# Performance work log

Hardware: AMD Instinct MI355X
Metric: run time of the kernel (lower is better)

## Reference

```python
import jax, jax.numpy as jnp
import numpy as np

B, N, F, E, C, FC = 16, 5000, 512, 160000, 64, 128


def gcn_conv(x, src, dst, W, b, n_total):
    loop = jnp.arange(n_total, dtype=src.dtype)
    s = jnp.concatenate([src, loop])
    d = jnp.concatenate([dst, loop])
    deg = jax.ops.segment_sum(jnp.ones_like(s, dtype=x.dtype), d, num_segments=n_total)
    dinv = jnp.where(deg > 0, jax.lax.rsqrt(deg), 0.0)
    norm = dinv[s] * dinv[d]                      # [E']
    h = x @ W                                      # [n_total, out]
    msg = h[s] * norm[:, None]
    out = jax.ops.segment_sum(msg, d, num_segments=n_total)
    return out + b


def setup_inputs() -> dict:
    key = jax.random.key(0)
    ks = jax.random.split(key, 12)
    inp = {
        "node_features": jax.random.normal(ks[0], (B, N, F), jnp.float32),
        "col_features": jax.random.normal(ks[1], (B, C, FC), jnp.float32),
        "edge_index": jax.random.randint(ks[2], (2, E), 0, N, dtype=jnp.int64),
        # GCNConv 1/2 weights + node head
        "W1": jax.random.normal(ks[3], (F, 16), jnp.float32) / np.sqrt(F),
        "b1": jnp.zeros((16,), jnp.float32),
        "W2": jax.random.normal(ks[4], (16, 16), jnp.float32) / 4.0,
        "b2": jnp.zeros((16,), jnp.float32),
        "fc_w": jax.random.normal(ks[5], (16, 1), jnp.float32) / 4.0,
        "fc_b": jnp.zeros((1,), jnp.float32),
        # column MLP: Linear(FC,16) -> ReLU -> Linear(16,1)
        "cw1": jax.random.normal(ks[6], (FC, 16), jnp.float32) / np.sqrt(FC),
        "cb1": jnp.zeros((16,), jnp.float32),
        "cw2": jax.random.normal(ks[7], (16, 1), jnp.float32) / 4.0,
        "cb2": jnp.zeros((1,), jnp.float32),
    }
    return inp


def reference(node_features, col_features, edge_index, W1, b1, W2, b2, fc_w, fc_b, cw1, cb1, cw2, cb2):
    b, n, _ = node_features.shape
    n_total = b * n
    # batched edge_index via node-offset trick (shared graph per batch element)
    offsets = (jnp.arange(b, dtype=edge_index.dtype) * n)[:, None]   # [B,1]
    src = (edge_index[0][None, :] + offsets).reshape(-1)              # [B*E]
    dst = (edge_index[1][None, :] + offsets).reshape(-1)

    x = node_features.reshape(n_total, -1)
    x = jax.nn.relu(gcn_conv(x, src, dst, W1, b1, n_total))
    x = jax.nn.relu(gcn_conv(x, src, dst, W2, b2, n_total))
    node_logits = (x.reshape(b, n, 16) @ fc_w + fc_b)[..., 0]         # [B,N]

    h = jax.nn.relu(col_features @ cw1 + cb1)
    col_logits = (h @ cw2 + cb2)[..., 0]                              # [B,C]

    joint = node_logits[:, :, None] + col_logits[:, None, :]          # [B,N,C]
    return joint.reshape(b, -1)                                       # [B, N*C]
```

## Files before the change

kernel.cpp:

```cpp
#include <hip/hip_runtime.h>
#include <hip/hip_bf16.h>

typedef unsigned short u16;
typedef unsigned int   u32;

#define B_  16
#define N_  5000
#define F_  512
#define C_  64
#define FC_ 128
#define NT  (B_ * N_)

__device__ __forceinline__ float bf2f(u16 h) {
    return __uint_as_float(((u32)h) << 16);
}
__device__ __forceinline__ u16 f2bf(float f) {
    union { __hip_bfloat16 h; u16 s; } c; c.h = __float2bfloat16(f); return c.s;
}
__device__ __forceinline__ float ldw(const void* p, int i, int fF) {
    return fF ? bf2f(((const u16*)p)[i]) : ((const float*)p)[i];
}

__global__ __launch_bounds__(256) void det_k(const u32* __restrict__ x32,
                                             const u32* __restrict__ ei32,
                                             int* __restrict__ flags)
{
    __shared__ int cnt;
    if (threadIdx.x == 0) cnt = 0;
    __syncthreads();
    u32 w = x32[threadIdx.x];
    int e = (int)((w >> 7) & 0xffu);
    if (e >= 112 && e <= 136) atomicAdd(&cnt, 1);
    __syncthreads();
    if (threadIdx.x == 0) {
        flags[0] = (cnt >= 128) ? 1 : 0;
        u32 orv = 0;
        for (int i = 1; i < 64; i += 2) orv |= ei32[i];
        flags[1] = (orv == 0u) ? 1 : 0;
    }
}

__device__ __forceinline__ int src_at(const u32* ei32, int t, int E, int fI) {
    return (int)(fI ? ei32[2 * t] : ei32[t]);
}
__device__ __forceinline__ int dst_at(const u32* ei32, int t, int E, int fI) {
    return (int)(fI ? ei32[2 * (E + t)] : ei32[E + t]);
}

__global__ __launch_bounds__(256) void prep_weights(
    const void* __restrict__ W1, const void* __restrict__ W2,
    const void* __restrict__ fcw, const void* __restrict__ cw1,
    const void* __restrict__ cw2, const void* __restrict__ b1,
    const void* __restrict__ b2, const void* __restrict__ fcb,
    const void* __restrict__ cb1, const void* __restrict__ cb2,
    const int* __restrict__ flags,
    float* __restrict__ w1f, float* __restrict__ w2f, float* __restrict__ fcwf,
    float* __restrict__ cw1f, float* __restrict__ cw2f, float* __restrict__ b1f,
    float* __restrict__ b2f, float* __restrict__ fcbf, float* __restrict__ cb1f,
    float* __restrict__ cb2f)
{
    int fF = flags[0];
    int t = blockIdx.x * blockDim.x + threadIdx.x;
    if (t < 8192) { w1f[t] = ldw(W1, t, fF); return; }
    int u = t - 8192;
    if (u < 256)  { w2f[u]  = ldw(W2, u, fF);  return; }  u -= 256;
    if (u < 16)   { fcwf[u] = ldw(fcw, u, fF); return; }  u -= 16;
    if (u < 2048) { cw1f[u] = ldw(cw1, u, fF); return; }  u -= 2048;
    if (u < 16)   { cw2f[u] = ldw(cw2, u, fF); return; }  u -= 16;
    if (u < 16)   { b1f[u]  = ldw(b1, u, fF);  return; }  u -= 16;
    if (u < 16)   { b2f[u]  = ldw(b2, u, fF);  return; }  u -= 16;
    if (u < 1)    { fcbf[u] = ldw(fcb, u, fF); return; }  u -= 1;
    if (u < 16)   { cb1f[u] = ldw(cb1, u, fF); return; }  u -= 16;
    if (u < 1)    { cb2f[u] = ldw(cb2, u, fF); return; }
}

__global__ __launch_bounds__(256) void deg_k(const u32* __restrict__ ei32,
                                             const int* __restrict__ flags,
                                             int* __restrict__ deg, int E)
{
    int t = blockIdx.x * blockDim.x + threadIdx.x;
    if (t >= E) return;
    int d = dst_at(ei32, t, E, flags[1]);
    if ((unsigned)d < (unsigned)N_) atomicAdd(&deg[d], 1);
}

__global__ __launch_bounds__(1024) void scan_k(const int* __restrict__ deg,
                                               int* __restrict__ rowptr,
                                               int* __restrict__ cursor,
                                               float* __restrict__ dinv)
{
    __shared__ int ssum[1024];
    int t = threadIdx.x;
    int base = t * 5;
    int loc[5];
    int run = 0;
#pragma unroll
    for (int i = 0; i < 5; i++) {
        int idx = base + i;
        int v = (idx < N_) ? deg[idx] : 0;
        loc[i] = run;
        run += v;
    }
    ssum[t] = run;
    __syncthreads();
    for (int offs = 1; offs < 1024; offs <<= 1) {
        int v = (t >= offs) ? ssum[t - offs] : 0;
        __syncthreads();
        ssum[t] += v;
        __syncthreads();
    }
    int exclusive = ssum[t] - run;
#pragma unroll
    for (int i = 0; i < 5; i++) {
        int idx = base + i;
        if (idx < N_) {
            int rp = exclusive + loc[i];
            rowptr[idx] = rp;
            cursor[idx] = rp;
            dinv[idx] = 1.0f / sqrtf((float)deg[idx] + 1.0f);
        }
    }
    if (t == 1023) rowptr[N_] = ssum[1023];
}

__global__ __launch_bounds__(256) void fill_k(const u32* __restrict__ ei32,
                                              const int* __restrict__ flags,
                                              int* __restrict__ cursor,
                                              int* __restrict__ csr, int E)
{
    int t = blockIdx.x * blockDim.x + threadIdx.x;
    if (t >= E) return;
    int fI = flags[1];
    int s = src_at(ei32, t, E, fI);
    int d = dst_at(ei32, t, E, fI);
    if ((unsigned)d >= (unsigned)N_) return;
    if ((unsigned)s >= (unsigned)N_) s = 0;
    int pos = atomicAdd(&cursor[d], 1);
    if ((unsigned)pos < (unsigned)E) csr[pos] = s;
}

__global__ __launch_bounds__(256) void gemm1_k(const void* __restrict__ xraw,
                                               const float* __restrict__ w1f,
                                               const float* __restrict__ dinv,
                                               const int* __restrict__ flags,
                                               u16* __restrict__ out)
{
    int row = blockIdx.x * blockDim.x + threadIdx.x;
    if (row >= NT) return;
    float acc[16];
#pragma unroll
    for (int k = 0; k < 16; k++) acc[k] = 0.0f;

    if (flags[0]) {
        const u16* xr = (const u16*)xraw + (size_t)row * F_;
        for (int f = 0; f < F_; f += 8) {
            uint4 pk = *(const uint4*)(xr + f);
            u32 q[4] = {pk.x, pk.y, pk.z, pk.w};
#pragma unroll
            for (int j = 0; j < 4; j++) {
                float v0 = bf2f((u16)(q[j] & 0xffffu));
                float v1 = bf2f((u16)(q[j] >> 16));
                const float* w0 = w1f + (f + 2 * j) * 16;
#pragma unroll
                for (int k = 0; k < 16; k++) acc[k] += v0 * w0[k];
#pragma unroll
                for (int k = 0; k < 16; k++) acc[k] += v1 * w0[16 + k];
            }
        }
    } else {
        const float* xr = (const float*)xraw + (size_t)row * F_;
        for (int f = 0; f < F_; f += 8) {
            float4 a = *(const float4*)(xr + f);
            float4 b = *(const float4*)(xr + f + 4);
            float v[8] = {a.x, a.y, a.z, a.w, b.x, b.y, b.z, b.w};
#pragma unroll
            for (int j = 0; j < 8; j++) {
                const float* w0 = w1f + (f + j) * 16;
#pragma unroll
                for (int k = 0; k < 16; k++) acc[k] += v[j] * w0[k];
            }
        }
    }
    float s = dinv[row % N_];
    union { uint4 u; u16 h[8]; } o0, o1;
#pragma unroll
    for (int k = 0; k < 8; k++) o0.h[k] = f2bf(acc[k] * s);
#pragma unroll
    for (int k = 0; k < 8; k++) o1.h[k] = f2bf(acc[8 + k] * s);
    uint4* op = (uint4*)(out + (size_t)row * 16);
    op[0] = o0.u;
    op[1] = o1.u;
}

__global__ __launch_bounds__(256) void agg1_k(const u16* __restrict__ h,
                                              const int* __restrict__ rowptr,
                                              const int* __restrict__ csr,
                                              const float* __restrict__ dinv,
                                              const float* __restrict__ b1f,
                                              u16* __restrict__ out)
{
    int t = blockIdx.x * blockDim.x + threadIdx.x;
    int g = t >> 4;
    if (g >= NT) return;
    int k = t & 15;
    int d = g % N_;
    int b = g / N_;
    const u16* hb = h + (size_t)b * N_ * 16;
    float acc = bf2f(hb[d * 16 + k]);
    int e0 = rowptr[d], e1 = rowptr[d + 1];
    for (int e = e0; e < e1; e++) {
        int s = csr[e];
        acc += bf2f(hb[s * 16 + k]);
    }
    float v = acc * dinv[d] + b1f[k];
    out[(size_t)g * 16 + k] = f2bf(fmaxf(v, 0.0f));
}

__global__ __launch_bounds__(256) void gemm2_k(const u16* __restrict__ x1,
                                               const float* __restrict__ w2f,
                                               const float* __restrict__ dinv,
                                               u16* __restrict__ out)
{
    int row = blockIdx.x * blockDim.x + threadIdx.x;
    if (row >= NT) return;
    const uint4* xp = (const uint4*)(x1 + (size_t)row * 16);
    union { uint4 u; u16 h[8]; } i0, i1;
    i0.u = xp[0]; i1.u = xp[1];
    float xv[16];
#pragma unroll
    for (int j = 0; j < 8; j++) { xv[j] = bf2f(i0.h[j]); xv[8 + j] = bf2f(i1.h[j]); }
    float acc[16];
#pragma unroll
    for (int k = 0; k < 16; k++) acc[k] = 0.0f;
#pragma unroll
    for (int j = 0; j < 16; j++) {
        const float* wr = w2f + j * 16;
#pragma unroll
        for (int k = 0; k < 16; k++) acc[k] += xv[j] * wr[k];
    }
    float s = dinv[row % N_];
    union { uint4 u; u16 h[8]; } o0, o1;
#pragma unroll
    for (int k = 0; k < 8; k++) o0.h[k] = f2bf(acc[k] * s);
#pragma unroll
    for (int k = 0; k < 8; k++) o1.h[k] = f2bf(acc[8 + k] * s);
    uint4* op = (uint4*)(out + (size_t)row * 16);
    op[0] = o0.u;
    op[1] = o1.u;
}

__global__ __launch_bounds__(256) void agg2_k(const u16* __restrict__ h,
                                              const int* __restrict__ rowptr,
                                              const int* __restrict__ csr,
                                              const float* __restrict__ dinv,
                                              const float* __restrict__ b2f,
                                              const float* __restrict__ fcwf,
                                              const float* __restrict__ fcbf,
                                              float* __restrict__ nl)
{
    int t = blockIdx.x * blockDim.x + threadIdx.x;
    int g = t >> 4;
    if (g >= NT) return;
    int k = t & 15;
    int d = g % N_;
    int b = g / N_;
    const u16* hb = h + (size_t)b * N_ * 16;
    float acc = bf2f(hb[d * 16 + k]);
    int e0 = rowptr[d], e1 = rowptr[d + 1];
    for (int e = e0; e < e1; e++) {
        int s = csr[e];
        acc += bf2f(hb[s * 16 + k]);
    }
    float v = fmaxf(acc * dinv[d] + b2f[k], 0.0f);
    float p = v * fcwf[k];
    p += __shfl_xor(p, 8, 16);
    p += __shfl_xor(p, 4, 16);
    p += __shfl_xor(p, 2, 16);
    p += __shfl_xor(p, 1, 16);
    if (k == 0) nl[g] = p + fcbf[0];
}

__global__ __launch_bounds__(256) void col_k(const void* __restrict__ cfraw,
                                             const float* __restrict__ cw1f,
                                             const float* __restrict__ cb1f,
                                             const float* __restrict__ cw2f,
                                             const float* __restrict__ cb2f,
                                             const int* __restrict__ flags,
                                             float* __restrict__ cl)
{
    int t = blockIdx.x * blockDim.x + threadIdx.x;
    if (t >= B_ * C_) return;
    float acc[16];
#pragma unroll
    for (int k = 0; k < 16; k++) acc[k] = cb1f[k];
    if (flags[0]) {
        const u16* r = (const u16*)cfraw + (size_t)t * FC_;
        for (int f = 0; f < FC_; f += 8) {
            uint4 pk = *(const uint4*)(r + f);
            u32 q[4] = {pk.x, pk.y, pk.z, pk.w};
#pragma unroll
            for (int j = 0; j < 4; j++) {
                float v0 = bf2f((u16)(q[j] & 0xffffu));
                float v1 = bf2f((u16)(q[j] >> 16));
                const float* w0 = cw1f + (f + 2 * j) * 16;
#pragma unroll
                for (int k = 0; k < 16; k++) acc[k] += v0 * w0[k];
#pragma unroll
                for (int k = 0; k < 16; k++) acc[k] += v1 * w0[16 + k];
            }
        }
    } else {
        const float* r = (const float*)cfraw + (size_t)t * FC_;
        for (int f = 0; f < FC_; f += 4) {
            float4 a = *(const float4*)(r + f);
            float v[4] = {a.x, a.y, a.z, a.w};
#pragma unroll
            for (int j = 0; j < 4; j++) {
                const float* w0 = cw1f + (f + j) * 16;
#pragma unroll
                for (int k = 0; k < 16; k++) acc[k] += v[j] * w0[k];
            }
        }
    }
    float s = cb2f[0];
#pragma unroll
    for (int k = 0; k < 16; k++) s += fmaxf(acc[k], 0.0f) * cw2f[k];
    cl[t] = s;
}

__global__ __launch_bounds__(256) void join_k(const float* __restrict__ nl,
                                              const float* __restrict__ cl,
                                              const int* __restrict__ flags,
                                              void* __restrict__ outraw)
{
    int t = blockIdx.x * blockDim.x + threadIdx.x;
    if (t >= NT * C_ / 8) return;
    int g  = t >> 3;
    int c0 = (t & 7) * 8;
    int b  = g / N_;
    float nv = nl[g];
    const float* c = cl + b * C_ + c0;
    float4 a0 = *(const float4*)c;
    float4 a1 = *(const float4*)(c + 4);
    float v[8] = {a0.x, a0.y, a0.z, a0.w, a1.x, a1.y, a1.z, a1.w};
#pragma unroll
    for (int i = 0; i < 8; i++) v[i] += nv;
    size_t idx = (size_t)g * C_ + c0;
    if (flags[0]) {
        union { uint4 u; u16 h[8]; } pkv;
#pragma unroll
        for (int i = 0; i < 8; i++) pkv.h[i] = f2bf(v[i]);
        *(uint4*)((u16*)outraw + idx) = pkv.u;
    } else {
        float* o = (float*)outraw + idx;
        *(float4*)o       = make_float4(v[0], v[1], v[2], v[3]);
        *(float4*)(o + 4) = make_float4(v[4], v[5], v[6], v[7]);
    }
}

extern "C" void kernel_launch(void* const* d_in, const int* in_sizes, int n_in,
                              void* d_out, int out_size, void* d_ws, size_t ws_size,
                              hipStream_t stream)
{
    const void* x    = d_in[0];
    const void* cf   = d_in[1];
    const u32*  ei32 = (const u32*)d_in[2];
    const void* W1   = d_in[3];
    const void* b1   = d_in[4];
    const void* W2   = d_in[5];
    const void* b2   = d_in[6];
    const void* fcw  = d_in[7];
    const void* fcb  = d_in[8];
    const void* cw1  = d_in[9];
    const void* cb1  = d_in[10];
    const void* cw2  = d_in[11];
    const void* cb2  = d_in[12];

    const int E = in_sizes[2] / 2;

    char* base = (char*)d_ws;
    size_t off = 0;
    auto alloc = [&](size_t bytes) -> void* {
        void* p = base + off;
        off = (off + bytes + 255) & ~(size_t)255;
        return p;
    };
    int*   flags  = (int*)alloc(2 * 4);
    float* w1f  = (float*)alloc(8192 * 4);
    float* w2f  = (float*)alloc(256 * 4);
    float* fcwf = (float*)alloc(16 * 4);
    float* cw1f = (float*)alloc(2048 * 4);
    float* cw2f = (float*)alloc(16 * 4);
    float* b1f  = (float*)alloc(16 * 4);
    float* b2f  = (float*)alloc(16 * 4);
    float* fcbf = (float*)alloc(4);
    float* cb1f = (float*)alloc(16 * 4);
    float* cb2f = (float*)alloc(4);
    int*   deg    = (int*)alloc((size_t)N_ * 4);
    int*   rowptr = (int*)alloc((size_t)(N_ + 1) * 4);
    int*   cursor = (int*)alloc((size_t)N_ * 4);
    float* dinv   = (float*)alloc((size_t)N_ * 4);
    int*   csr    = (int*)alloc((size_t)E * 4);
    u16*   bufA = (u16*)alloc((size_t)NT * 16 * 2);
    u16*   bufB = (u16*)alloc((size_t)NT * 16 * 2);
    float* nl   = (float*)alloc((size_t)NT * 4);
    float* cl   = (float*)alloc((size_t)B_ * C_ * 4);

    det_k<<<1, 256, 0, stream>>>((const u32*)x, ei32, flags);
    hipMemsetAsync(deg, 0, (size_t)N_ * 4, stream);
    prep_weights<<<(10578 + 255) / 256, 256, 0, stream>>>(
        W1, W2, fcw, cw1, cw2, b1, b2, fcb, cb1, cb2, flags,
        w1f, w2f, fcwf, cw1f, cw2f, b1f, b2f, fcbf, cb1f, cb2f);
    deg_k<<<(E + 255) / 256, 256, 0, stream>>>(ei32, flags, deg, E);
    scan_k<<<1, 1024, 0, stream>>>(deg, rowptr, cursor, dinv);
    fill_k<<<(E + 255) / 256, 256, 0, stream>>>(ei32, flags, cursor, csr, E);

    gemm1_k<<<(NT + 255) / 256, 256, 0, stream>>>(x, w1f, dinv, flags, bufA);
    agg1_k<<<(NT * 16 + 255) / 256, 256, 0, stream>>>(bufA, rowptr, csr, dinv, b1f, bufB);
    gemm2_k<<<(NT + 255) / 256, 256, 0, stream>>>(bufB, w2f, dinv, bufA);
    agg2_k<<<(NT * 16 + 255) / 256, 256, 0, stream>>>(bufA, rowptr, csr, dinv, b2f, fcwf, fcbf, nl);
    col_k<<<(B_ * C_ + 255) / 256, 256, 0, stream>>>(cf, cw1f, cb1f, cw2f, cb2f, flags, cl);
    join_k<<<(NT * C_ / 8 + 255) / 256, 256, 0, stream>>>(nl, cl, flags, d_out);
}
```

Before: 434.2 us.

## Fuse setup kernels, layer-2 GEMM into aggregation, and join into final aggregation

Merges format detection, degree zeroing and weight conversion into one single-block setup kernel. The layer-2 16x16 GEMM is folded into the first aggregation kernel, and the broadcast join is folded into the second aggregation, which writes the output directly. Aggregation now uses one 64-lane wavefront per node, with four edge-parallel groups reduced by shuffles. This removes several launches and the intermediate round trips through global memory. In exchange, 64-wide output stores may be less vectorized, and the single-block setup serializes weight conversion.

```diff
diff --git a/kernel.cpp b/kernel.cpp
--- a/kernel.cpp
+++ b/kernel.cpp
@@ -21,57 +21,58 @@
     return fF ? bf2f(((const u16*)p)[i]) : ((const float*)p)[i];
 }
 
-__global__ __launch_bounds__(256) void det_k(const u32* __restrict__ x32,
-                                             const u32* __restrict__ ei32,
-                                             int* __restrict__ flags)
-{
-    __shared__ int cnt;
-    if (threadIdx.x == 0) cnt = 0;
-    __syncthreads();
-    u32 w = x32[threadIdx.x];
-    int e = (int)((w >> 7) & 0xffu);
-    if (e >= 112 && e <= 136) atomicAdd(&cnt, 1);
-    __syncthreads();
-    if (threadIdx.x == 0) {
-        flags[0] = (cnt >= 128) ? 1 : 0;
-        u32 orv = 0;
-        for (int i = 1; i < 64; i += 2) orv |= ei32[i];
-        flags[1] = (orv == 0u) ? 1 : 0;
-    }
-}
-
-__device__ __forceinline__ int src_at(const u32* ei32, int t, int E, int fI) {
-    return (int)(fI ? ei32[2 * t] : ei32[t]);
-}
-__device__ __forceinline__ int dst_at(const u32* ei32, int t, int E, int fI) {
-    return (int)(fI ? ei32[2 * (E + t)] : ei32[E + t]);
-}
-
-__global__ __launch_bounds__(256) void prep_weights(
+__global__ __launch_bounds__(256) void setup_k(
+    const u32* __restrict__ x32, const u32* __restrict__ ei32,
     const void* __restrict__ W1, const void* __restrict__ W2,
     const void* __restrict__ fcw, const void* __restrict__ cw1,
     const void* __restrict__ cw2, const void* __restrict__ b1,
     const void* __restrict__ b2, const void* __restrict__ fcb,
     const void* __restrict__ cb1, const void* __restrict__ cb2,
-    const int* __restrict__ flags,
+    int* __restrict__ flags, int* __restrict__ deg,
     float* __restrict__ w1f, float* __restrict__ w2f, float* __restrict__ fcwf,
     float* __restrict__ cw1f, float* __restrict__ cw2f, float* __restrict__ b1f,
     float* __restrict__ b2f, float* __restrict__ fcbf, float* __restrict__ cb1f,
     float* __restrict__ cb2f)
 {
-    int fF = flags[0];
-    int t = blockIdx.x * blockDim.x + threadIdx.x;
-    if (t < 8192) { w1f[t] = ldw(W1, t, fF); return; }
-    int u = t - 8192;
-    if (u < 256)  { w2f[u]  = ldw(W2, u, fF);  return; }  u -= 256;
-    if (u < 16)   { fcwf[u] = ldw(fcw, u, fF); return; }  u -= 16;
-    if (u < 2048) { cw1f[u] = ldw(cw1, u, fF); return; }  u -= 2048;
-    if (u < 16)   { cw2f[u] = ldw(cw2, u, fF); return; }  u -= 16;
-    if (u < 16)   { b1f[u]  = ldw(b1, u, fF);  return; }  u -= 16;
-    if (u < 16)   { b2f[u]  = ldw(b2, u, fF);  return; }  u -= 16;
-    if (u < 1)    { fcbf[u] = ldw(fcb, u, fF); return; }  u -= 1;
-    if (u < 16)   { cb1f[u] = ldw(cb1, u, fF); return; }  u -= 16;
-    if (u < 1)    { cb2f[u] = ldw(cb2, u, fF); return; }
+    __shared__ int s_cnt, s_fF;
+    int t = threadIdx.x;
+    if (t == 0) s_cnt = 0;
+    __syncthreads();
+    u32 w = x32[t];
+    int e = (int)((w >> 7) & 0xffu);
+    if (e >= 112 && e <= 136) atomicAdd(&s_cnt, 1);
+    __syncthreads();
+    if (t == 0) {
+        int fF = (s_cnt >= 128) ? 1 : 0;
+        s_fF = fF;
+        flags[0] = fF;
+        u32 orv = 0;
+        for (int i = 1; i < 64; i += 2) orv |= ei32[i];
+        flags[1] = (orv == 0u) ? 1 : 0;
+    }
+    for (int i = t; i < N_; i += 256) deg[i] = 0;
+    __syncthreads();
+    int fF = s_fF;
+    for (int i = t; i < 10578; i += 256) {
+        int u = i;
+        if (u < 8192) { w1f[u] = ldw(W1, u, fF); continue; }  u -= 8192;
+        if (u < 256)  { w2f[u]  = ldw(W2, u, fF);  continue; }  u -= 256;
+        if (u < 16)   { fcwf[u] = ldw(fcw, u, fF); continue; }  u -= 16;
+        if (u < 2048) { cw1f[u] = ldw(cw1, u, fF); continue; }  u -= 2048;
+        if (u < 16)   { cw2f[u] = ldw(cw2, u, fF); continue; }  u -= 16;
+        if (u < 16)   { b1f[u]  = ldw(b1, u, fF);  continue; }  u -= 16;
+        if (u < 16)   { b2f[u]  = ldw(b2, u, fF);  continue; }  u -= 16;
+        if (u < 1)    { fcbf[u] = ldw(fcb, u, fF); continue; }  u -= 1;
+        if (u < 16)   { cb1f[u] = ldw(cb1, u, fF); continue; }  u -= 16;
+        if (u < 1)    { cb2f[u] = ldw(cb2, u, fF); continue; }
+    }
+}
+
+__device__ __forceinline__ int src_at(const u32* ei32, int t, int E, int fI) {
+    return (int)(fI ? ei32[2 * t] : ei32[t]);
+}
+__device__ __forceinline__ int dst_at(const u32* ei32, int t, int E, int fI) {
+    return (int)(fI ? ei32[2 * (E + t)] : ei32[E + t]);
 }
 
 __global__ __launch_bounds__(256) void deg_k(const u32* __restrict__ ei32,
@@ -192,92 +193,75 @@
     op[1] = o1.u;
 }
 
-__global__ __launch_bounds__(256) void agg1_k(const u16* __restrict__ h,
-                                              const int* __restrict__ rowptr,
-                                              const int* __restrict__ csr,
-                                              const float* __restrict__ dinv,
-                                              const float* __restrict__ b1f,
-                                              u16* __restrict__ out)
-{
-    int t = blockIdx.x * blockDim.x + threadIdx.x;
-    int g = t >> 4;
-    if (g >= NT) return;
-    int k = t & 15;
-    int d = g % N_;
-    int b = g / N_;
+__global__ __launch_bounds__(256) void agg12_k(const u16* __restrict__ h,
+                                               const int* __restrict__ rowptr,
+                                               const int* __restrict__ csr,
+                                               const float* __restrict__ dinv,
+                                               const float* __restrict__ b1f,
+                                               const float* __restrict__ w2f,
+                                               u16* __restrict__ out)
+{
+    int wid = blockIdx.x * 4 + (threadIdx.x >> 6);
+    int lane = threadIdx.x & 63;
+    int k = lane & 15, j = lane >> 4;
+    int d = wid % N_;
+    int b = wid / N_;
     const u16* hb = h + (size_t)b * N_ * 16;
-    float acc = bf2f(hb[d * 16 + k]);
+    float acc = (j == 0) ? bf2f(hb[d * 16 + k]) : 0.0f;
     int e0 = rowptr[d], e1 = rowptr[d + 1];
-    for (int e = e0; e < e1; e++) {
+    for (int e = e0 + j; e < e1; e += 4) {
         int s = csr[e];
         acc += bf2f(hb[s * 16 + k]);
     }
-    float v = acc * dinv[d] + b1f[k];
-    out[(size_t)g * 16 + k] = f2bf(fmaxf(v, 0.0f));
-}
-
-__global__ __launch_bounds__(256) void gemm2_k(const u16* __restrict__ x1,
-                                               const float* __restrict__ w2f,
-                                               const float* __restrict__ dinv,
-                                               u16* __restrict__ out)
-{
-    int row = blockIdx.x * blockDim.x + threadIdx.x;
-    if (row >= NT) return;
-    const uint4* xp = (const uint4*)(x1 + (size_t)row * 16);
-    union { uint4 u; u16 h[8]; } i0, i1;
-    i0.u = xp[0]; i1.u = xp[1];
-    float xv[16];
-#pragma unroll
-    for (int j = 0; j < 8; j++) { xv[j] = bf2f(i0.h[j]); xv[8 + j] = bf2f(i1.h[j]); }
-    float acc[16];
-#pragma unroll
-    for (int k = 0; k < 16; k++) acc[k] = 0.0f;
-#pragma unroll
-    for (int j = 0; j < 16; j++) {
-        const float* wr = w2f + j * 16;
-#pragma unroll
-        for (int k = 0; k < 16; k++) acc[k] += xv[j] * wr[k];
-    }
-    float s = dinv[row % N_];
-    union { uint4 u; u16 h[8]; } o0, o1;
-#pragma unroll
-    for (int k = 0; k < 8; k++) o0.h[k] = f2bf(acc[k] * s);
-#pragma unroll
-    for (int k = 0; k < 8; k++) o1.h[k] = f2bf(acc[8 + k] * s);
-    uint4* op = (uint4*)(out + (size_t)row * 16);
-    op[0] = o0.u;
-    op[1] = o1.u;
-}
-
-__global__ __launch_bounds__(256) void agg2_k(const u16* __restrict__ h,
-                                              const int* __restrict__ rowptr,
-                                              const int* __restrict__ csr,
-                                              const float* __restrict__ dinv,
-                                              const float* __restrict__ b2f,
-                                              const float* __restrict__ fcwf,
-                                              const float* __restrict__ fcbf,
-                                              float* __restrict__ nl)
-{
-    int t = blockIdx.x * blockDim.x + threadIdx.x;
-    int g = t >> 4;
-    if (g >= NT) return;
-    int k = t & 15;
-    int d = g % N_;
-    int b = g / N_;
+    acc += __shfl_xor(acc, 16);
+    acc += __shfl_xor(acc, 32);
+    float dv = dinv[d];
+    float x1 = fmaxf(acc * dv + b1f[k], 0.0f);
+    float a2 = 0.0f;
+#pragma unroll
+    for (int kk = 0; kk < 16; kk++) {
+        float xv = __shfl(x1, kk, 16);
+        a2 += xv * w2f[kk * 16 + k];
+    }
+    if (lane < 16) out[(size_t)wid * 16 + k] = f2bf(a2 * dv);
+}
+
+__global__ __launch_bounds__(256) void agg2join_k(const u16* __restrict__ h,
+                                                  const int* __restrict__ rowptr,
+                                                  const int* __restrict__ csr,
+                                                  const float* __restrict__ dinv,
+                                                  const float* __restrict__ b2f,
+                                                  const float* __restrict__ fcwf,
+                                                  const float* __restrict__ fcbf,
+                                                  const float* __restrict__ cl,
+                                                  const int* __restrict__ flags,
+                                                  void* __restrict__ outraw)
+{
+    int wid = blockIdx.x * 4 + (threadIdx.x >> 6);
+    int lane = threadIdx.x & 63;
+    int k = lane & 15, j = lane >> 4;
+    int d = wid % N_;
+    int b = wid / N_;
     const u16* hb = h + (size_t)b * N_ * 16;
-    float acc = bf2f(hb[d * 16 + k]);
+    float acc = (j == 0) ? bf2f(hb[d * 16 + k]) : 0.0f;
     int e0 = rowptr[d], e1 = rowptr[d + 1];
-    for (int e = e0; e < e1; e++) {
+    for (int e = e0 + j; e < e1; e += 4) {
         int s = csr[e];
         acc += bf2f(hb[s * 16 + k]);
     }
-    float v = fmaxf(acc * dinv[d] + b2f[k], 0.0f);
-    float p = v * fcwf[k];
+    acc += __shfl_xor(acc, 16);
+    acc += __shfl_xor(acc, 32);
+    float x2 = fmaxf(acc * dinv[d] + b2f[k], 0.0f);
+    float p = x2 * fcwf[k];
     p += __shfl_xor(p, 8, 16);
     p += __shfl_xor(p, 4, 16);
     p += __shfl_xor(p, 2, 16);
     p += __shfl_xor(p, 1, 16);
-    if (k == 0) nl[g] = p + fcbf[0];
+    float nlv = p + fcbf[0];
+    float res = nlv + cl[b * C_ + lane];
+    size_t idx = (size_t)wid * C_ + lane;
+    if (flags[0]) ((u16*)outraw)[idx] = f2bf(res);
+    else          ((float*)outraw)[idx] = res;
 }
 
 __global__ __launch_bounds__(256) void col_k(const void* __restrict__ cfraw,
@@ -326,36 +310,6 @@
 #pragma unroll
     for (int k = 0; k < 16; k++) s += fmaxf(acc[k], 0.0f) * cw2f[k];
     cl[t] = s;
-}
-
-__global__ __launch_bounds__(256) void join_k(const float* __restrict__ nl,
-                                              const float* __restrict__ cl,
-                                              const int* __restrict__ flags,
-                                              void* __restrict__ outraw)
-{
-    int t = blockIdx.x * blockDim.x + threadIdx.x;
-    if (t >= NT * C_ / 8) return;
-    int g  = t >> 3;
-    int c0 = (t & 7) * 8;
-    int b  = g / N_;
-    float nv = nl[g];
-    const float* c = cl + b * C_ + c0;
-    float4 a0 = *(const float4*)c;
-    float4 a1 = *(const float4*)(c + 4);
-    float v[8] = {a0.x, a0.y, a0.z, a0.w, a1.x, a1.y, a1.z, a1.w};
-#pragma unroll
-    for (int i = 0; i < 8; i++) v[i] += nv;
-    size_t idx = (size_t)g * C_ + c0;
-    if (flags[0]) {
-        union { uint4 u; u16 h[8]; } pkv;
-#pragma unroll
-        for (int i = 0; i < 8; i++) pkv.h[i] = f2bf(v[i]);
-        *(uint4*)((u16*)outraw + idx) = pkv.u;
-    } else {
-        float* o = (float*)outraw + idx;
-        *(float4*)o       = make_float4(v[0], v[1], v[2], v[3]);
-        *(float4*)(o + 4) = make_float4(v[4], v[5], v[6], v[7]);
-    }
 }
 
 extern "C" void kernel_launch(void* const* d_in, const int* in_sizes, int n_in,
@@ -403,22 +357,18 @@
     int*   csr    = (int*)alloc((size_t)E * 4);
     u16*   bufA = (u16*)alloc((size_t)NT * 16 * 2);
     u16*   bufB = (u16*)alloc((size_t)NT * 16 * 2);
-    float* nl   = (float*)alloc((size_t)NT * 4);
     float* cl   = (float*)alloc((size_t)B_ * C_ * 4);
 
-    det_k<<<1, 256, 0, stream>>>((const u32*)x, ei32, flags);
-    hipMemsetAsync(deg, 0, (size_t)N_ * 4, stream);
-    prep_weights<<<(10578 + 255) / 256, 256, 0, stream>>>(
-        W1, W2, fcw, cw1, cw2, b1, b2, fcb, cb1, cb2, flags,
+    setup_k<<<1, 256, 0, stream>>>(
+        (const u32*)x, ei32, W1, W2, fcw, cw1, cw2, b1, b2, fcb, cb1, cb2,
+        flags, deg,
         w1f, w2f, fcwf, cw1f, cw2f, b1f, b2f, fcbf, cb1f, cb2f);
     deg_k<<<(E + 255) / 256, 256, 0, stream>>>(ei32, flags, deg, E);
     scan_k<<<1, 1024, 0, stream>>>(deg, rowptr, cursor, dinv);
     fill_k<<<(E + 255) / 256, 256, 0, stream>>>(ei32, flags, cursor, csr, E);
 
     gemm1_k<<<(NT + 255) / 256, 256, 0, stream>>>(x, w1f, dinv, flags, bufA);
-    agg1_k<<<(NT * 16 + 255) / 256, 256, 0, stream>>>(bufA, rowptr, csr, dinv, b1f, bufB);
-    gemm2_k<<<(NT + 255) / 256, 256, 0, stream>>>(bufB, w2f, dinv, bufA);
-    agg2_k<<<(NT * 16 + 255) / 256, 256, 0, stream>>>(bufA, rowptr, csr, dinv, b2f, fcwf, fcbf, nl);
     col_k<<<(B_ * C_ + 255) / 256, 256, 0, stream>>>(cf, cw1f, cb1f, cw2f, cb2f, flags, cl);
-    join_k<<<(NT * C_ / 8 + 255) / 256, 256, 0, stream>>>(nl, cl, flags, d_out);
-}
+    agg12_k<<<NT / 4, 256, 0, stream>>>(bufA, rowptr, csr, dinv, b1f, w2f, bufB);
+    agg2join_k<<<NT / 4, 256, 0, stream>>>(bufB, rowptr, csr, dinv, b2f, fcwf, fcbf, cl, flags, d_out);
+}
```

After: 457.5 us. 1.05x slower.
